# Kernel tuning notes

Measured on AMD Instinct MI355X. Metric: run time of the kernel, lower is better.

## Reference

```python
import jax, jax.numpy as jnp
import numpy as np

NUM_HEADS = 12
INV_SQRT_DK = 0.125  # 1/sqrt(64)

def setup_inputs() -> dict:
    key = jax.random.key(0)
    ks = jax.random.split(key, 5)
    B, N, C = 32, 577, 768
    s = 0.02
    return {
        "x": jax.random.normal(ks[0], (B, N, C), dtype=jnp.float32),
        "W_qkv": jax.random.normal(ks[1], (C, 3 * C), dtype=jnp.float32) * s,
        "b_qkv": jax.random.normal(ks[2], (3 * C,), dtype=jnp.float32) * s,
        "W_proj": jax.random.normal(ks[3], (C, C), dtype=jnp.float32) * s,
        "b_proj": jax.random.normal(ks[4], (C,), dtype=jnp.float32) * s,
    }

def reference(x, W_qkv, b_qkv, W_proj, b_proj):
    B, N, C = x.shape
    H = NUM_HEADS
    Dh = C // H
    # qkv projection: [B,N,3C] -> [3,B,H,N,Dh]
    qkv = (x @ W_qkv + b_qkv).reshape(B, N, 3, H, Dh).transpose(2, 0, 3, 1, 4)
    q, k, v = qkv[0], qkv[1], qkv[2]
    # scaled dot-product attention, scores [B,H,N,N]
    attn = jnp.einsum("bhnd,bhmd->bhnm", q, k) * INV_SQRT_DK
    attn = jax.nn.softmax(attn, axis=-1)
    # attn_drop: rate 0 -> identity (eval)
    out = jnp.einsum("bhnm,bhmd->bhnd", attn, v)  # [B,H,N,Dh]
    out = out.transpose(0, 2, 1, 3).reshape(B, N, C)
    out = out @ W_proj + b_proj
    # proj_drop: rate 0 -> identity (eval)
    return out
```

## Files before the change

kernel.cpp:

```cpp
#include <hip/hip_runtime.h>
#include <stdint.h>

typedef __attribute__((ext_vector_type(8))) short short8;
typedef __attribute__((ext_vector_type(4))) short short4v;
typedef __attribute__((ext_vector_type(4))) float f32x4;

#define MFMA(a,b,c) __builtin_amdgcn_mfma_f32_16x16x32_bf16((a),(b),(c),0,0,0)
#define QSCALE 0.18033688f
#define VT_LD 584
#define NTOK 577
#define PT_LD 72
#define AS1 __attribute__((address_space(1)))
#define AS3 __attribute__((address_space(3)))

__device__ __forceinline__ unsigned short f2bf(float f) {
    unsigned int u = __float_as_uint(f);
    u += 0x7fffu + ((u >> 16) & 1u);
    return (unsigned short)(u >> 16);
}
__device__ __forceinline__ float bf2f(unsigned short u) {
    return __uint_as_float(((unsigned int)u) << 16);
}
__device__ __forceinline__ unsigned int cvt_pk_bf16(float lo, float hi) {
    unsigned int r;
    asm("v_cvt_pk_bf16_f32 %0, %1, %2" : "=v"(r) : "v"(lo), "v"(hi));
    return r;
}

__global__ __launch_bounds__(256) void cvt_f32_bf16(const float* __restrict__ in,
                                                    unsigned short* __restrict__ out, int n4) {
    int i = blockIdx.x * 256 + threadIdx.x;
    if (i < n4) {
        float4 v = ((const float4*)in)[i];
        short4v s;
        s[0] = (short)f2bf(v.x); s[1] = (short)f2bf(v.y);
        s[2] = (short)f2bf(v.z); s[3] = (short)f2bf(v.w);
        ((short4v*)out)[i] = s;
    }
}

__global__ __launch_bounds__(256) void transpose_cvt(const float* __restrict__ in,
                                                     unsigned short* __restrict__ out,
                                                     int R, int C) {
    __shared__ float tile[32][33];
    int c0 = blockIdx.x * 32, r0 = blockIdx.y * 32;
    int lc = threadIdx.x & 31, lr = threadIdx.x >> 5;
    #pragma unroll
    for (int i = 0; i < 4; ++i) {
        int r = lr + i * 8;
        tile[r][lc] = in[(size_t)(r0 + r) * C + c0 + lc];
    }
    __syncthreads();
    #pragma unroll
    for (int i = 0; i < 4; ++i) {
        int r = lr + i * 8;
        out[(size_t)(c0 + r) * R + r0 + lc] = f2bf(tile[lc][r]);
    }
}

template<int EPI>
__global__ __launch_bounds__(512) void gemm256x128(
    const unsigned short* __restrict__ A,
    const unsigned short* __restrict__ Bt,
    const float* __restrict__ bias,
    unsigned short* __restrict__ q_out, unsigned short* __restrict__ k_out,
    unsigned short* __restrict__ vt_out, float* __restrict__ f_out,
    int M, int NB)
{
    __shared__ __align__(16) unsigned short As[256 * 64];
    __shared__ __align__(16) unsigned short Bs[128 * 64];

    const int nwg = gridDim.x, orig = blockIdx.x;
    const int qd = nwg >> 3, r8 = nwg & 7;
    const int xcd = orig & 7, j = orig >> 3;
    const int wg = (xcd < r8 ? xcd * (qd + 1) : r8 * (qd + 1) + (xcd - r8) * qd) + j;
    const int bx = wg % NB, by = wg / NB;
    const int m0 = by * 256, n0 = bx * 128;

    const int t = threadIdx.x, lane = t & 63, w = t >> 6;
    const int g = lane >> 4, c = lane & 15;
    const int wr = w >> 1, wcn = w & 1;
    const int srow = t >> 3;
    const int csw = (((t & 7) ^ (srow & 7)) * 8);

    f32x4 acc[4][4] = {};

    for (int k0 = 0; k0 < 768; k0 += 64) {
        #pragma unroll
        for (int i = 0; i < 4; ++i) {
            int row = i * 64 + srow;
            int ra = m0 + row; ra = ra < M ? ra : M - 1;
            __builtin_amdgcn_global_load_lds(
                (const AS1 unsigned int*)&A[(size_t)ra * 768 + k0 + csw],
                (AS3 unsigned int*)&As[i * 4096 + w * 512], 16, 0, 0);
        }
        #pragma unroll
        for (int i = 0; i < 2; ++i) {
            int row = i * 64 + srow;
            __builtin_amdgcn_global_load_lds(
                (const AS1 unsigned int*)&Bt[(size_t)(n0 + row) * 768 + k0 + csw],
                (AS3 unsigned int*)&Bs[i * 4096 + w * 512], 16, 0, 0);
        }
        __syncthreads();
        #pragma unroll
        for (int kk = 0; kk < 2; ++kk) {
            short8 af[4], bfv[4];
            #pragma unroll
            for (int mf = 0; mf < 4; ++mf) {
                int rr = wr * 64 + mf * 16 + c;
                af[mf] = *(const short8*)&As[rr * 64 + (((kk * 4 + g) ^ (c & 7)) * 8)];
            }
            #pragma unroll
            for (int nf = 0; nf < 4; ++nf) {
                int rr = wcn * 64 + nf * 16 + c;
                bfv[nf] = *(const short8*)&Bs[rr * 64 + (((kk * 4 + g) ^ (c & 7)) * 8)];
            }
            __builtin_amdgcn_s_setprio(1);
            #pragma unroll
            for (int mf = 0; mf < 4; ++mf)
            #pragma unroll
            for (int nf = 0; nf < 4; ++nf)
                acc[mf][nf] = MFMA(af[mf], bfv[nf], acc[mf][nf]);
            __builtin_amdgcn_s_setprio(0);
        }
        __syncthreads();
    }

    #pragma unroll
    for (int mf = 0; mf < 4; ++mf)
    #pragma unroll
    for (int nf = 0; nf < 4; ++nf) {
        int n = n0 + wcn * 64 + nf * 16 + c;
        float bv = bias[n];
        #pragma unroll
        for (int e = 0; e < 4; ++e) {
            int m = m0 + wr * 64 + mf * 16 + g * 4 + e;
            if (m >= M) continue;
            float v = acc[mf][nf][e] + bv;
            if (EPI == 0) {
                int which = n / 768;
                int rr = n - which * 768;
                int h = rr >> 6, d = rr & 63;
                int b = m / 577, tok = m - b * 577;
                int bh = b * 12 + h;
                if (which == 0)      q_out[((size_t)bh * 577 + tok) * 64 + d] = f2bf(v * QSCALE);
                else if (which == 1) k_out[((size_t)bh * 577 + tok) * 64 + d] = f2bf(v);
                else                 vt_out[((size_t)bh * 64 + d) * VT_LD + tok] = f2bf(v);
            } else {
                f_out[(size_t)m * 768 + n] = v;
            }
        }
    }
}

template<int EPI>
__global__ __launch_bounds__(256) void gemm128(
    const unsigned short* __restrict__ A,
    const unsigned short* __restrict__ Bt,
    const float* __restrict__ bias,
    unsigned short* __restrict__ q_out, unsigned short* __restrict__ k_out,
    unsigned short* __restrict__ vt_out, float* __restrict__ f_out,
    int M, int K, int NB)
{
    __shared__ __align__(16) unsigned short As[128 * 64];
    __shared__ __align__(16) unsigned short Bs[128 * 64];

    const int nwg = gridDim.x, orig = blockIdx.x;
    const int qd = nwg >> 3, r = nwg & 7;
    const int xcd = orig & 7, j = orig >> 3;
    const int wg = (xcd < r ? xcd * (qd + 1) : r * (qd + 1) + (xcd - r) * qd) + j;
    const int bx = wg % NB, by = wg / NB;
    const int m0 = by * 128, n0 = bx * 128;

    const int t = threadIdx.x, lane = t & 63, w = t >> 6;
    const int g = lane >> 4, c = lane & 15;
    const int wr = w >> 1, wc = w & 1;
    const int rowi = t >> 3;
    const int csw = (((t & 7) ^ (rowi & 7)) * 8);

    f32x4 acc[4][4] = {};

    for (int k0 = 0; k0 < K; k0 += 64) {
        #pragma unroll
        for (int i = 0; i < 4; ++i) {
            int row = i * 32 + rowi;
            int ra = m0 + row; ra = ra < M ? ra : M - 1;
            __builtin_amdgcn_global_load_lds(
                (const AS1 unsigned int*)&A[(size_t)ra * K + k0 + csw],
                (AS3 unsigned int*)&As[(i * 256 + w * 64) * 8], 16, 0, 0);
            __builtin_amdgcn_global_load_lds(
                (const AS1 unsigned int*)&Bt[(size_t)(n0 + row) * K + k0 + csw],
                (AS3 unsigned int*)&Bs[(i * 256 + w * 64) * 8], 16, 0, 0);
        }
        __syncthreads();
        #pragma unroll
        for (int kk = 0; kk < 2; ++kk) {
            short8 af[4], bfr[4];
            #pragma unroll
            for (int mf = 0; mf < 4; ++mf) {
                int rr = wr * 64 + mf * 16 + c;
                af[mf] = *(const short8*)&As[rr * 64 + (((kk * 4 + g) ^ (c & 7)) * 8)];
            }
            #pragma unroll
            for (int nf = 0; nf < 4; ++nf) {
                int rr = wc * 64 + nf * 16 + c;
                bfr[nf] = *(const short8*)&Bs[rr * 64 + (((kk * 4 + g) ^ (c & 7)) * 8)];
            }
            __builtin_amdgcn_s_setprio(1);
            #pragma unroll
            for (int mf = 0; mf < 4; ++mf)
            #pragma unroll
            for (int nf = 0; nf < 4; ++nf)
                acc[mf][nf] = MFMA(af[mf], bfr[nf], acc[mf][nf]);
            __builtin_amdgcn_s_setprio(0);
        }
        __syncthreads();
    }

    #pragma unroll
    for (int mf = 0; mf < 4; ++mf)
    #pragma unroll
    for (int nf = 0; nf < 4; ++nf) {
        int n = n0 + wc * 64 + nf * 16 + c;
        float bv = bias[n];
        #pragma unroll
        for (int e = 0; e < 4; ++e) {
            int m = m0 + wr * 64 + mf * 16 + g * 4 + e;
            if (m >= M) continue;
            float v = acc[mf][nf][e] + bv;
            if (EPI == 0) {
                int which = n / 768;
                int rr = n - which * 768;
                int h = rr >> 6, d = rr & 63;
                int b = m / 577, tok = m - b * 577;
                int bh = b * 12 + h;
                if (which == 0)      q_out[((size_t)bh * 577 + tok) * 64 + d] = f2bf(v * QSCALE);
                else if (which == 1) k_out[((size_t)bh * 577 + tok) * 64 + d] = f2bf(v);
                else                 vt_out[((size_t)bh * 64 + d) * VT_LD + tok] = f2bf(v);
            } else {
                f_out[(size_t)m * 768 + n] = v;
            }
        }
    }
}

__global__ __launch_bounds__(256, 3) void attn_flash(
    const unsigned short* __restrict__ Qg,
    const unsigned short* __restrict__ Kg,
    const unsigned short* __restrict__ Vtg,
    unsigned short* __restrict__ Og)
{
    __shared__ __align__(16) unsigned short KL[2][64][64];
    __shared__ __align__(16) unsigned short VL[2][64][64];
    __shared__ __align__(16) unsigned short pt[4][16][PT_LD];

    const int nwg = gridDim.x, orig = blockIdx.x;
    const int qd = nwg >> 3, jj8 = nwg & 7;
    const int xcd = orig & 7, jj = orig >> 3;
    const int wgid = (xcd < jj8 ? xcd * (qd + 1) : jj8 * (qd + 1) + (xcd - jj8) * qd) + jj;
    const int qt = wgid % 10;
    const int bh = wgid / 10;
    const int b = bh / 12, h = bh - b * 12;
    const int t = threadIdx.x, w = t >> 6, lane = t & 63;
    const int g = lane >> 4, c = lane & 15;
    const int rowi = t >> 3;
    const int gch = ((t & 7) ^ (rowi & 7)) * 8;

    const unsigned short* Qh = Qg + (size_t)bh * NTOK * 64;
    const unsigned short* Kh = Kg + (size_t)bh * NTOK * 64;
    const unsigned short* Vh = Vtg + (size_t)bh * 64 * VT_LD;

    const int q = qt * 64 + w * 16 + c;
    const int qc = q < NTOK ? q : NTOK - 1;

    short8 bq0 = *(const short8*)&Qh[(size_t)qc * 64 +      g * 8];
    short8 bq1 = *(const short8*)&Qh[(size_t)qc * 64 + 32 + g * 8];

    auto stage = [&](int buf, int kbase) {
        #pragma unroll
        for (int i = 0; i < 2; ++i) {
            __builtin_amdgcn_global_load_lds(
                (const AS1 unsigned int*)&Kh[(size_t)(kbase + i * 32 + rowi) * 64 + gch],
                (AS3 unsigned int*)(&KL[buf][0][0] + (i * 256 + w * 64) * 8), 16, 0, 0);
            __builtin_amdgcn_global_load_lds(
                (const AS1 unsigned int*)&Vh[(size_t)(i * 32 + rowi) * VT_LD + kbase + gch],
                (AS3 unsigned int*)(&VL[buf][0][0] + (i * 256 + w * 64) * 8), 16, 0, 0);
        }
    };

    f32x4 lsumv = {};
    f32x4 ot[4] = {};

    stage(0, 0);
    __syncthreads();

    int cur = 0;
    for (int kt = 0; kt < 9; ++kt) {
        if (kt < 8) stage(cur ^ 1, (kt + 1) * 64);
        short8 kf0[4], kf1[4];
        #pragma unroll
        for (int f = 0; f < 4; ++f) {
            const unsigned short* kr = &KL[cur][f * 16 + c][0];
            kf0[f] = *(const short8*)&kr[((g    ) ^ (c & 7)) * 8];
            kf1[f] = *(const short8*)&kr[((4 + g) ^ (c & 7)) * 8];
        }
        f32x4 st[4];
        __builtin_amdgcn_s_setprio(1);
        #pragma unroll
        for (int f = 0; f < 4; ++f) {
            f32x4 z = {};
            z = MFMA(kf0[f], bq0, z);
            z = MFMA(kf1[f], bq1, z);
            st[f] = z;
        }
        __builtin_amdgcn_s_setprio(0);
        #pragma unroll
        for (int f = 0; f < 4; ++f) {
            float p0 = exp2f(fminf(st[f][0], 60.f));
            float p1 = exp2f(fminf(st[f][1], 60.f));
            float p2 = exp2f(fminf(st[f][2], 60.f));
            float p3 = exp2f(fminf(st[f][3], 60.f));
            lsumv[0] += p0; lsumv[1] += p1; lsumv[2] += p2; lsumv[3] += p3;
            uint2 pw;
            pw.x = cvt_pk_bf16(p0, p1);
            pw.y = cvt_pk_bf16(p2, p3);
            *(uint2*)&pt[w][c][f * 16 + g * 4] = pw;
        }
        __builtin_amdgcn_s_setprio(1);
        #pragma unroll
        for (int kk = 0; kk < 2; ++kk) {
            short8 bp = *(const short8*)&pt[w][c][kk * 32 + g * 8];
            #pragma unroll
            for (int df = 0; df < 4; ++df) {
                const unsigned short* vr = &VL[cur][df * 16 + c][0];
                short8 av = *(const short8*)&vr[((kk * 4 + g) ^ (c & 7)) * 8];
                ot[df] = MFMA(av, bp, ot[df]);
            }
        }
        __builtin_amdgcn_s_setprio(0);
        __syncthreads();
        cur ^= 1;
    }

    float lsum = (lsumv[0] + lsumv[1]) + (lsumv[2] + lsumv[3]);
    lsum += __shfl_xor(lsum, 16);
    lsum += __shfl_xor(lsum, 32);

    {
        const unsigned short* kp = &Kh[(size_t)576 * 64];
        float dot = 0.f;
        #pragma unroll
        for (int jx = 0; jx < 8; ++jx) {
            dot += bf2f((unsigned short)bq0[jx]) * bf2f(kp[g * 8 + jx]);
            dot += bf2f((unsigned short)bq1[jx]) * bf2f(kp[32 + g * 8 + jx]);
        }
        dot += __shfl_xor(dot, 16);
        dot += __shfl_xor(dot, 32);
        float p = exp2f(fminf(dot, 60.f));
        lsum += p;
        #pragma unroll
        for (int df = 0; df < 4; ++df)
        #pragma unroll
        for (int e = 0; e < 4; ++e)
            ot[df][e] += p * bf2f(Vh[(size_t)(df * 16 + g * 4 + e) * VT_LD + 576]);
    }

    float inv = 1.0f / lsum;
    if (q < NTOK) {
        size_t orow = ((size_t)b * NTOK + q) * 768 + h * 64;
        #pragma unroll
        for (int df = 0; df < 4; ++df) {
            uint2 ov;
            ov.x = cvt_pk_bf16(ot[df][0] * inv, ot[df][1] * inv);
            ov.y = cvt_pk_bf16(ot[df][2] * inv, ot[df][3] * inv);
            *(uint2*)&Og[orow + df * 16 + g * 4] = ov;
        }
    }
}

extern "C" void kernel_launch(void* const* d_in, const int* in_sizes, int n_in,
                              void* d_out, int out_size, void* d_ws, size_t ws_size,
                              hipStream_t stream) {
    const float* x      = (const float*)d_in[0];
    const float* W_qkv  = (const float*)d_in[1];
    const float* b_qkv  = (const float*)d_in[2];
    const float* W_proj = (const float*)d_in[3];
    const float* b_proj = (const float*)d_in[4];
    float* out = (float*)d_out;

    const int B = 32, N = 577, C = 768, H = 12;
    const int M = B * N;

    char* ws = (char*)d_ws;
    size_t off = 0;
    auto alloc = [&](size_t bytes) {
        char* p = ws + off;
        off += (bytes + 255) & ~(size_t)255;
        return p;
    };
    unsigned short* xb    = (unsigned short*)alloc((size_t)M * C * 2);
    unsigned short* wqkvt = (unsigned short*)alloc((size_t)3 * C * C * 2);
    unsigned short* wprjt = (unsigned short*)alloc((size_t)C * C * 2);
    unsigned short* Qb    = (unsigned short*)alloc((size_t)B * H * N * 64 * 2);
    unsigned short* Kb    = (unsigned short*)alloc((size_t)B * H * N * 64 * 2);
    unsigned short* Vtb   = (unsigned short*)alloc((size_t)B * H * 64 * VT_LD * 2);
    unsigned short* attn  = xb;

    int n4 = M * C / 4;
    cvt_f32_bf16<<<dim3((n4 + 255) / 256), 256, 0, stream>>>(x, xb, n4);
    transpose_cvt<<<dim3(3 * C / 32, C / 32), 256, 0, stream>>>(W_qkv, wqkvt, C, 3 * C);
    transpose_cvt<<<dim3(C / 32, C / 32), 256, 0, stream>>>(W_proj, wprjt, C, C);

    gemm256x128<0><<<dim3(73 * 18), 512, 0, stream>>>(
        xb, wqkvt, b_qkv, Qb, Kb, Vtb, nullptr, M, 18);

    attn_flash<<<dim3(3840), 256, 0, stream>>>(Qb, Kb, Vtb, attn);

    gemm128<1><<<dim3(6 * 145), 256, 0, stream>>>(
        attn, wprjt, b_proj, nullptr, nullptr, nullptr, out, M, C, 6);
}
```

Measured before the change: 247.0 us.

## Rewrite QKV GEMM as per-wave-private double-buffered pipeline without block barriers

The QKV projection GEMM now uses 128x128 tiles with 256 threads, and each wave loads its own private A and B sub-tiles into LDS. This removes the __syncthreads calls in the K loop. Loads are double-buffered with explicit vmcnt/lgkmcnt waits so the next K-tile's global-to-LDS copy overlaps the MFMAs on the current one. The cost is redundant loads, because waves sharing rows or columns each fetch their own copy. It also doubles the grid size and relies on hand-tuned waitcnt counts that must match the number of issued loads.

After: 337.3 us. 1.37x slower.

```diff
diff --git a/kernel.cpp b/kernel.cpp
--- a/kernel.cpp
+++ b/kernel.cpp
@@ -59,7 +59,7 @@
 }
 
 template<int EPI>
-__global__ __launch_bounds__(512) void gemm256x128(
+__global__ __launch_bounds__(256, 1) void gemm_wp(
     const unsigned short* __restrict__ A,
     const unsigned short* __restrict__ Bt,
     const float* __restrict__ bias,
@@ -67,63 +67,74 @@
     unsigned short* __restrict__ vt_out, float* __restrict__ f_out,
     int M, int NB)
 {
-    __shared__ __align__(16) unsigned short As[256 * 64];
-    __shared__ __align__(16) unsigned short Bs[128 * 64];
+    __shared__ __align__(16) unsigned short AL[4][2][64 * 64];
+    __shared__ __align__(16) unsigned short BL[4][2][64 * 64];
 
     const int nwg = gridDim.x, orig = blockIdx.x;
     const int qd = nwg >> 3, r8 = nwg & 7;
-    const int xcd = orig & 7, j = orig >> 3;
-    const int wg = (xcd < r8 ? xcd * (qd + 1) : r8 * (qd + 1) + (xcd - r8) * qd) + j;
+    const int xcd = orig & 7, j0 = orig >> 3;
+    const int wg = (xcd < r8 ? xcd * (qd + 1) : r8 * (qd + 1) + (xcd - r8) * qd) + j0;
     const int bx = wg % NB, by = wg / NB;
-    const int m0 = by * 256, n0 = bx * 128;
+    const int m0 = by * 128, n0 = bx * 128;
 
     const int t = threadIdx.x, lane = t & 63, w = t >> 6;
     const int g = lane >> 4, c = lane & 15;
     const int wr = w >> 1, wcn = w & 1;
-    const int srow = t >> 3;
-    const int csw = (((t & 7) ^ (srow & 7)) * 8);
+    const int l8 = lane >> 3;
+    const int csw = (((lane & 7) ^ l8) * 8);
+    const int rch = (c & 7);
 
     f32x4 acc[4][4] = {};
 
-    for (int k0 = 0; k0 < 768; k0 += 64) {
-        #pragma unroll
-        for (int i = 0; i < 4; ++i) {
-            int row = i * 64 + srow;
-            int ra = m0 + row; ra = ra < M ? ra : M - 1;
-            __builtin_amdgcn_global_load_lds(
-                (const AS1 unsigned int*)&A[(size_t)ra * 768 + k0 + csw],
-                (AS3 unsigned int*)&As[i * 4096 + w * 512], 16, 0, 0);
-        }
-        #pragma unroll
-        for (int i = 0; i < 2; ++i) {
-            int row = i * 64 + srow;
-            __builtin_amdgcn_global_load_lds(
-                (const AS1 unsigned int*)&Bt[(size_t)(n0 + row) * 768 + k0 + csw],
-                (AS3 unsigned int*)&Bs[i * 4096 + w * 512], 16, 0, 0);
-        }
-        __syncthreads();
+    auto stage = [&](int buf, int kt) {
+        const int k0 = kt * 64;
+        #pragma unroll
+        for (int jj = 0; jj < 8; ++jj) {
+            int arow = m0 + wr * 64 + jj * 8 + l8;
+            arow = arow < M ? arow : M - 1;
+            __builtin_amdgcn_global_load_lds(
+                (const AS1 unsigned int*)&A[(size_t)arow * 768 + k0 + csw],
+                (AS3 unsigned int*)&AL[w][buf][jj * 512], 16, 0, 0);
+            int brow = n0 + wcn * 64 + jj * 8 + l8;
+            __builtin_amdgcn_global_load_lds(
+                (const AS1 unsigned int*)&Bt[(size_t)brow * 768 + k0 + csw],
+                (AS3 unsigned int*)&BL[w][buf][jj * 512], 16, 0, 0);
+        }
+    };
+
+    stage(0, 0);
+    stage(1, 1);
+    asm volatile("s_waitcnt vmcnt(16)" ::: "memory");
+    __builtin_amdgcn_sched_barrier(0);
+
+    #pragma unroll
+    for (int kt = 0; kt < 12; ++kt) {
+        const int buf = kt & 1;
+        short8 af[2][4], bfv[2][4];
         #pragma unroll
         for (int kk = 0; kk < 2; ++kk) {
-            short8 af[4], bfv[4];
-            #pragma unroll
-            for (int mf = 0; mf < 4; ++mf) {
-                int rr = wr * 64 + mf * 16 + c;
-                af[mf] = *(const short8*)&As[rr * 64 + (((kk * 4 + g) ^ (c & 7)) * 8)];
-            }
-            #pragma unroll
-            for (int nf = 0; nf < 4; ++nf) {
-                int rr = wcn * 64 + nf * 16 + c;
-                bfv[nf] = *(const short8*)&Bs[rr * 64 + (((kk * 4 + g) ^ (c & 7)) * 8)];
-            }
-            __builtin_amdgcn_s_setprio(1);
             #pragma unroll
             for (int mf = 0; mf < 4; ++mf)
+                af[kk][mf] = *(const short8*)&AL[w][buf][(mf * 16 + c) * 64 + (((kk * 4 + g) ^ rch) * 8)];
             #pragma unroll
             for (int nf = 0; nf < 4; ++nf)
-                acc[mf][nf] = MFMA(af[mf], bfv[nf], acc[mf][nf]);
-            __builtin_amdgcn_s_setprio(0);
-        }
-        __syncthreads();
+                bfv[kk][nf] = *(const short8*)&BL[w][buf][(nf * 16 + c) * 64 + (((kk * 4 + g) ^ rch) * 8)];
+        }
+        asm volatile("s_waitcnt lgkmcnt(0)" ::: "memory");
+        __builtin_amdgcn_sched_barrier(0);
+        if (kt <= 9) stage(buf, kt + 2);
+        __builtin_amdgcn_s_setprio(1);
+        #pragma unroll
+        for (int kk = 0; kk < 2; ++kk)
+        #pragma unroll
+        for (int mf = 0; mf < 4; ++mf)
+        #pragma unroll
+        for (int nf = 0; nf < 4; ++nf)
+            acc[mf][nf] = MFMA(af[kk][mf], bfv[kk][nf], acc[mf][nf]);
+        __builtin_amdgcn_s_setprio(0);
+        if (kt <= 9)       asm volatile("s_waitcnt vmcnt(16)" ::: "memory");
+        else if (kt == 10) asm volatile("s_waitcnt vmcnt(0)" ::: "memory");
+        __builtin_amdgcn_sched_barrier(0);
     }
 
     #pragma unroll
@@ -411,7 +422,7 @@
     transpose_cvt<<<dim3(3 * C / 32, C / 32), 256, 0, stream>>>(W_qkv, wqkvt, C, 3 * C);
     transpose_cvt<<<dim3(C / 32, C / 32), 256, 0, stream>>>(W_proj, wprjt, C, C);
 
-    gemm256x128<0><<<dim3(73 * 18), 512, 0, stream>>>(
+    gemm_wp<0><<<dim3(145 * 18), 256, 0, stream>>>(
         xb, wqkvt, b_qkv, Qb, Kb, Vtb, nullptr, M, 18);
 
     attn_flash<<<dim3(3840), 256, 0, stream>>>(Qb, Kb, Vtb, attn);
```
